# Optimization experiments

Hardware: AMD Instinct MI355X
Metric: run time of the kernel (lower is better)

The kernel has to match this reference:

```python
import jax, jax.numpy as jnp
import numpy as np

DIM = 1024
HEADS = 16


def setup_inputs() -> dict:
    key = jax.random.key(0)
    k1, k2, k3, k4 = jax.random.split(key, 4)
    x = jax.random.normal(k1, (4, 2048, DIM), dtype=jnp.float32)
    s = 1.0 / np.sqrt(DIM)
    w_qkv = jax.random.normal(k2, (DIM, 3 * DIM), dtype=jnp.float32) * s
    w_out = jax.random.normal(k3, (DIM, DIM), dtype=jnp.float32) * s
    b_out = jax.random.normal(k4, (DIM,), dtype=jnp.float32) * 0.01
    return {"x": x, "w_qkv": w_qkv, "w_out": w_out, "b_out": b_out}


def reference(x, w_qkv, w_out, b_out):
    b, n, d = x.shape
    h = HEADS
    dh = d // h
    scale = dh ** -0.5
    qkv = x @ w_qkv  # [b, n, 3d]
    q, k, v = jnp.split(qkv, 3, axis=-1)
    # [b, n, d] -> [b, h, n, dh]
    def to_heads(t):
        return t.reshape(b, n, h, dh).transpose(0, 2, 1, 3)
    q, k, v = to_heads(q), to_heads(k), to_heads(v)
    dots = jnp.einsum('bhid,bhjd->bhij', q, k) * scale
    attn = jax.nn.softmax(dots, axis=-1)
    out = jnp.einsum('bhij,bhjd->bhid', attn, v)
    out = out.transpose(0, 2, 1, 3).reshape(b, n, d)
    return out @ w_out + b_out
```

## Files before the change

kernel.cpp:

```cpp
#include <hip/hip_runtime.h>
#include <hip/hip_bf16.h>


typedef __attribute__((ext_vector_type(4))) float f32x4;
typedef __attribute__((ext_vector_type(16))) float f32x16;
typedef __attribute__((ext_vector_type(8))) unsigned short u16x8;
typedef __attribute__((ext_vector_type(4))) unsigned short u16x4;
typedef __attribute__((ext_vector_type(4))) unsigned int u32x4;
typedef __attribute__((ext_vector_type(8))) __bf16 bf16x8;

static __device__ __forceinline__ f32x4 mfma_bf16(u16x8 a, u16x8 b, f32x4 c) {
    return __builtin_amdgcn_mfma_f32_16x16x32_bf16(
        __builtin_bit_cast(bf16x8, a), __builtin_bit_cast(bf16x8, b), c, 0, 0, 0);
}
static __device__ __forceinline__ f32x16 mfma32(u16x8 a, u16x8 b, f32x16 c) {
    return __builtin_amdgcn_mfma_f32_32x32x16_bf16(
        __builtin_bit_cast(bf16x8, a), __builtin_bit_cast(bf16x8, b), c, 0, 0, 0);
}

static __device__ __forceinline__ unsigned short f2bf(float f) {
    unsigned int u = __builtin_bit_cast(unsigned int, f);
    u += 0x7fffu + ((u >> 16) & 1u);
    return (unsigned short)(u >> 16);
}
static __device__ __forceinline__ unsigned int cvt_pk_bf16(float a, float b) {
    unsigned int r;
    asm("v_cvt_pk_bf16_f32 %0, %1, %2" : "=v"(r) : "v"(a), "v"(b));
    return r;
}
static __device__ __forceinline__ float fexp2(float x) {
    float r;
    asm("v_exp_f32 %0, %1" : "=v"(r) : "v"(x));
    return r;
}
static __device__ __forceinline__ float frcp(float x) {
    float r;
    asm("v_rcp_f32 %0, %1" : "=v"(r) : "v"(x));
    return r;
}
typedef const __attribute__((address_space(1))) unsigned int* gp1_t;
typedef __attribute__((address_space(3))) unsigned int* lp3_t;
static __device__ __forceinline__ void gl_lds16(const void* g, void* l) {
    __builtin_amdgcn_global_load_lds((gp1_t)g, (lp3_t)l, 16, 0, 0);
}

__global__ void k_prep(const float* __restrict__ x, unsigned short* __restrict__ xb,
                       const float* __restrict__ w_qkv, unsigned short* __restrict__ wqkvT,
                       const float* __restrict__ w_out, unsigned short* __restrict__ woutT) {
    int blk = blockIdx.x, tid = threadIdx.x;
    if (blk < 2048) {
        int i = blk * 256 + tid;
        int stride = 2048 * 256;
        int n4 = 8192 * 1024 / 4;
        for (; i < n4; i += stride) {
            f32x4 v = ((const f32x4*)x)[i];
            u16x4 o;
            #pragma unroll
            for (int j = 0; j < 4; ++j) o[j] = f2bf(v[j]);
            ((u16x4*)xb)[i] = o;
        }
        return;
    }
    __shared__ float tile[32][33];
    const float* in; unsigned short* out; int R, C, scale_rows, c0, r0;
    float scale;
    if (blk < 5120) {
        int idx = blk - 2048;
        in = w_qkv; out = wqkvT; R = 1024; C = 3072;
        scale_rows = 1024; scale = 0.18033688f;
        c0 = (idx % 96) * 32; r0 = (idx / 96) * 32;
    } else {
        int idx = blk - 5120;
        in = w_out; out = woutT; R = 1024; C = 1024;
        scale_rows = 0; scale = 1.0f;
        c0 = (idx % 32) * 32; r0 = (idx / 32) * 32;
    }
    int tx = tid & 31, ty = tid >> 5;
    #pragma unroll
    for (int i = ty; i < 32; i += 8)
        tile[i][tx] = in[(size_t)(r0 + i) * C + c0 + tx];
    __syncthreads();
    #pragma unroll
    for (int i = ty; i < 32; i += 8) {
        float v = tile[tx][i];
        if (c0 + i < scale_rows) v *= scale;
        out[(size_t)(c0 + i) * R + r0 + tx] = f2bf(v);
    }
}

__global__ __launch_bounds__(512, 1) void k_gemm1f(
    const unsigned short* __restrict__ A,
    const unsigned short* __restrict__ BT,
    unsigned short* __restrict__ qkv,
    unsigned short* __restrict__ VTs)
{
    __shared__ unsigned short As[2][256 * 64];
    __shared__ unsigned short Bs[2][384 * 64];
    const int K = 1024;
    const int tid = threadIdx.x, lane = tid & 63, wave = tid >> 6;

    int lin = blockIdx.y * 8 + blockIdx.x;
    int xcd = lin & 7, idx = lin >> 3;
    int by = xcd * 4 + (idx >> 3);
    int bxg = idx & 7;
    const int m0 = by * 256, n0 = bxg * 384;

    const int wm = (wave >> 1) * 64, wn = (wave & 1) * 192;
    const int lr = lane & 15, half = lane >> 4;
    const int srow = lane >> 3, sslot = lane & 7;

    auto stage = [&](int buf, int t) {
        int k0 = t * 64;
        #pragma unroll
        for (int r = 0; r < 4; ++r) {
            int chunk = r * 8 + wave;
            int row = chunk * 8 + srow;
            int koff = (sslot ^ (row & 7)) * 8;
            gl_lds16(&A[(size_t)(m0 + row) * K + k0 + koff], &As[buf][chunk * 512]);
        }
        #pragma unroll
        for (int r = 0; r < 6; ++r) {
            int chunk = r * 8 + wave;
            int row = chunk * 8 + srow;
            int koff = (sslot ^ (row & 7)) * 8;
            gl_lds16(&BT[(size_t)(n0 + row) * K + k0 + koff], &Bs[buf][chunk * 512]);
        }
    };

    f32x4 acc[4][12] = {};

    stage(0, 0);
    asm volatile("s_waitcnt vmcnt(0)" ::: "memory");
    __builtin_amdgcn_s_barrier();

    for (int t = 0; t < 16; ++t) {
        const int cur = t & 1;
        if (t < 15) stage(cur ^ 1, t + 1);
        const unsigned short* Ab = As[cur];
        const unsigned short* Bb = Bs[cur];

        #pragma unroll
        for (int ks = 0; ks < 2; ++ks) {
            u16x8 af[4];
            #pragma unroll
            for (int i = 0; i < 4; ++i) {
                int ra = wm + i * 16 + lr;
                af[i] = *(const u16x8*)&Ab[ra * 64 + (((ks * 4 + half) ^ (ra & 7)) * 8)];
            }
            #pragma unroll
            for (int j = 0; j < 12; ++j) {
                int rb = wn + j * 16 + lr;
                u16x8 bfr = *(const u16x8*)&Bb[rb * 64 + (((ks * 4 + half) ^ (rb & 7)) * 8)];
                __builtin_amdgcn_s_setprio(1);
                #pragma unroll
                for (int i = 0; i < 4; ++i)
                    acc[i][j] = mfma_bf16(af[i], bfr, acc[i][j]);
                __builtin_amdgcn_s_setprio(0);
            }
        }

        asm volatile("s_waitcnt vmcnt(0) lgkmcnt(0)" ::: "memory");
        __builtin_amdgcn_s_barrier();
    }

    #pragma unroll
    for (int i = 0; i < 4; ++i) {
        int rowb = m0 + wm + i * 16 + half * 4;
        #pragma unroll
        for (int j = 0; j < 12; ++j) {
            int col = n0 + wn + j * 16 + lr;
            if (col < 2048) {
                #pragma unroll
                for (int r = 0; r < 4; ++r)
                    qkv[(size_t)(rowb + r) * 3072 + col] = f2bf(acc[i][j][r]);
            } else {
                int cj = col - 2048, h = cj >> 6, d = cj & 63;
                int b = rowb >> 11, n = rowb & 2047;
                u16x4 p;
                #pragma unroll
                for (int r = 0; r < 4; ++r) p[r] = f2bf(acc[i][j][r]);
                *(u16x4*)&VTs[((size_t)((b * 16 + h) * 64 + d)) * 2048 + n] = p;
            }
        }
    }
}

__global__ __launch_bounds__(512, 1) void k_gemm2(
    const unsigned short* __restrict__ A,
    const unsigned short* __restrict__ BT,
    const float* __restrict__ bias,
    float* __restrict__ outf)
{
    __shared__ unsigned short As[3][256 * 64];
    __shared__ unsigned short Bs[3][128 * 64];
    const int K = 1024;
    const int tid = threadIdx.x, lane = tid & 63, wave = tid >> 6;

    int lin = blockIdx.y * 8 + blockIdx.x;
    int virt = (lin & 7) * 32 + (lin >> 3);
    int bx = virt % 8, by = virt / 8;
    const int m0 = by * 256, n0 = bx * 128;

    const int wm = (wave >> 1) * 64, wn = (wave & 1) * 64;
    const int lr = lane & 15, half = lane >> 4;
    const int srow = lane >> 3, sslot = lane & 7;

    auto stage_sub = [&](int buf, int t, int h) {
        int k0 = t * 64;
        #pragma unroll
        for (int r = 0; r < 2; ++r) {
            int chunk = (h * 2 + r) * 8 + wave;
            int row = chunk * 8 + srow;
            int koff = (sslot ^ (row & 7)) * 8;
            gl_lds16(&A[(size_t)(m0 + row) * K + k0 + koff], &As[buf][chunk * 512]);
        }
        {
            int chunk = h * 8 + wave;
            int row = chunk * 8 + srow;
            int koff = (sslot ^ (row & 7)) * 8;
            gl_lds16(&BT[(size_t)(n0 + row) * K + k0 + koff], &Bs[buf][chunk * 512]);
        }
    };

    f32x4 acc[4][4] = {};

    stage_sub(0, 0, 0); stage_sub(0, 0, 1);
    stage_sub(1, 1, 0); stage_sub(1, 1, 1);
    asm volatile("s_waitcnt vmcnt(6)" ::: "memory");
    __builtin_amdgcn_s_barrier();

    for (int t = 0; t < 16; ++t) {
        const int cur = t % 3, nxt = (t + 2) % 3;
        const bool do_stage = (t + 2) < 16;
        const unsigned short* Ab = As[cur];
        const unsigned short* Bb = Bs[cur];

        #pragma unroll
        for (int ks = 0; ks < 2; ++ks) {
            u16x8 af[4], bfr[4];
            #pragma unroll
            for (int i = 0; i < 4; ++i) {
                int ra = wm + i * 16 + lr;
                af[i] = *(const u16x8*)&Ab[ra * 64 + (((ks * 4 + half) ^ (ra & 7)) * 8)];
                int rb = wn + i * 16 + lr;
                bfr[i] = *(const u16x8*)&Bb[rb * 64 + (((ks * 4 + half) ^ (rb & 7)) * 8)];
            }
            if (do_stage) stage_sub(nxt, t + 2, ks);
            if (ks == 1) {
                if (t < 14)       asm volatile("s_waitcnt vmcnt(6)" ::: "memory");
                else if (t == 14) asm volatile("s_waitcnt vmcnt(0)" ::: "memory");
            }
            __builtin_amdgcn_s_barrier();
            asm volatile("s_waitcnt lgkmcnt(0)" ::: "memory");
            __builtin_amdgcn_sched_barrier(0);
            __builtin_amdgcn_s_setprio(1);
            #pragma unroll
            for (int i = 0; i < 4; ++i)
                #pragma unroll
                for (int j = 0; j < 4; ++j)
                    acc[i][j] = mfma_bf16(af[i], bfr[j], acc[i][j]);
            __builtin_amdgcn_s_setprio(0);
            __builtin_amdgcn_s_barrier();
        }
    }

    #pragma unroll
    for (int i = 0; i < 4; ++i)
        #pragma unroll
        for (int j = 0; j < 4; ++j)
            #pragma unroll
            for (int r = 0; r < 4; ++r) {
                int row = m0 + wm + i * 16 + half * 4 + r;
                int col = n0 + wn + j * 16 + lr;
                outf[(size_t)row * 1024 + col] = acc[i][j][r] + bias[col];
            }
}

__global__ __launch_bounds__(256, 4) void k_attn(
    const unsigned short* __restrict__ qkv,
    const unsigned short* __restrict__ VTs,
    unsigned short* __restrict__ attn)
{
    __shared__ unsigned short Kt[2][64 * 64];
    __shared__ unsigned short Vt[2][64 * 64];
    const int tid = threadIdx.x, lane = tid & 63, wave = tid >> 6;

    int lin = blockIdx.y * 16 + blockIdx.x;
    int virt = (lin & 7) * 128 + (lin >> 3);
    int bh = virt >> 4;
    int q0 = (virt & 15) * 128 + wave * 32;

    const int lq = lane & 31;
    const int hi = lane >> 5;

    int b = bh >> 4, h = bh & 15;
    const unsigned short* Kq = qkv + (size_t)(b * 2048) * 3072 + 1024 + h * 64;
    const unsigned short* Vbase = VTs + (size_t)bh * 64 * 2048;

    u16x8 qf[4];
    {
        const unsigned short* Qr = qkv + (size_t)(b * 2048 + q0 + lq) * 3072 + h * 64;
        #pragma unroll
        for (int kk = 0; kk < 4; ++kk)
            qf[kk] = *(const u16x8*)&Qr[kk * 16 + hi * 8];
    }

    const int srow_in = lane >> 4, sslot = lane & 15;
    auto stage = [&](int buf, int j0) {
        #pragma unroll
        for (int c = 0; c < 2; ++c) {
            int chunk = wave * 2 + c;
            int row = chunk * 4 + srow_in;
            int v = sslot ^ (row & 15);
            int high = v >> 3, dsl = (v & 7) * 8;
            gl_lds16(Kq + (size_t)(j0 + high * 32 + row) * 3072 + dsl, &Kt[buf][chunk * 512]);
            gl_lds16(Vbase + (size_t)(high * 32 + row) * 2048 + j0 + dsl, &Vt[buf][chunk * 512]);
        }
    };

    f32x16 o[2] = {};
    f32x16 osum = {};
    const u16x8 onesf = {0x3F80, 0x3F80, 0x3F80, 0x3F80, 0x3F80, 0x3F80, 0x3F80, 0x3F80};

    stage(0, 0);
    __syncthreads();
    int cur = 0;

    for (int t = 0; t < 32; ++t) {
        if (t < 31) stage(cur ^ 1, (t + 1) * 64);

        f32x16 sacc[2] = {};
        __builtin_amdgcn_s_setprio(1);
        #pragma unroll
        for (int jb = 0; jb < 2; ++jb) {
            u16x8 kf[4];
            #pragma unroll
            for (int kk = 0; kk < 4; ++kk) {
                int s = (jb * 8 + kk * 2 + hi) ^ (lq & 15);
                kf[kk] = *(const u16x8*)&Kt[cur][lq * 128 + s * 8];
            }
            #pragma unroll
            for (int kk = 0; kk < 4; ++kk)
                sacc[jb] = mfma32(kf[kk], qf[kk], sacc[jb]);
        }
        __builtin_amdgcn_s_setprio(0);

        unsigned int pk[16];
        #pragma unroll
        for (int jb = 0; jb < 2; ++jb)
            #pragma unroll
            for (int i = 0; i < 8; ++i)
                pk[jb * 8 + i] = cvt_pk_bf16(fexp2(sacc[jb][2 * i]), fexp2(sacc[jb][2 * i + 1]));

        __builtin_amdgcn_s_setprio(1);
        #pragma unroll
        for (int kk = 0; kk < 4; ++kk) {
            const int base = (kk >> 1) * 8 + (kk & 1) * 4;
            unsigned int w0 = pk[base + 0], w2 = pk[base + 2];
            unsigned int w1 = pk[base + 1], w3 = pk[base + 3];
            asm("v_permlane32_swap_b32 %0, %1" : "+v"(w0), "+v"(w2));
            asm("v_permlane32_swap_b32 %0, %1" : "+v"(w1), "+v"(w3));
            u32x4 w; w[0] = w0; w[1] = w1; w[2] = w2; w[3] = w3;
            u16x8 pa = __builtin_bit_cast(u16x8, w);
            osum = mfma32(pa, onesf, osum);
            #pragma unroll
            for (int db = 0; db < 2; ++db) {
                int s = (db * 8 + kk * 2 + hi) ^ (lq & 15);
                u16x8 vf = *(const u16x8*)&Vt[cur][lq * 128 + s * 8];
                o[db] = mfma32(pa, vf, o[db]);
            }
        }
        __builtin_amdgcn_s_setprio(0);

        __syncthreads();
        cur ^= 1;
    }

    #pragma unroll
    for (int r = 0; r < 16; ++r) {
        int qrow = (r & 3) + 8 * (r >> 2) + 4 * hi;
        float invr = frcp(osum[r]);
        size_t ro = (size_t)(b * 2048 + q0 + qrow) * 1024 + h * 64;
        attn[ro + lq]      = f2bf(o[0][r] * invr);
        attn[ro + 32 + lq] = f2bf(o[1][r] * invr);
    }
}

extern "C" void kernel_launch(void* const* d_in, const int* in_sizes, int n_in,
                              void* d_out, int out_size, void* d_ws, size_t ws_size,
                              hipStream_t stream) {
    const float* x     = (const float*)d_in[0];
    const float* w_qkv = (const float*)d_in[1];
    const float* w_out = (const float*)d_in[2];
    const float* b_out = (const float*)d_in[3];
    float* out = (float*)d_out;

    char* ws = (char*)d_ws;
    size_t off = 0;
    auto alloc = [&](size_t bytes) -> void* {
        void* p = ws + off;
        off += (bytes + 255) & ~(size_t)255;
        return p;
    };
    unsigned short* xb    = (unsigned short*)alloc(8192ull * 1024 * 2);
    unsigned short* wqkvT = (unsigned short*)alloc(3072ull * 1024 * 2);
    unsigned short* woutT = (unsigned short*)alloc(1024ull * 1024 * 2);
    unsigned short* qkv   = (unsigned short*)alloc(8192ull * 3072 * 2);
    unsigned short* VTs   = (unsigned short*)alloc(64ull * 2048 * 64 * 2);
    if (off > ws_size) return;

    k_prep<<<6144, 256, 0, stream>>>(x, xb, w_qkv, wqkvT, w_out, woutT);
    k_gemm1f<<<dim3(8, 32), 512, 0, stream>>>(xb, wqkvT, qkv, VTs);
    k_attn<<<dim3(16, 64), 256, 0, stream>>>(qkv, VTs, xb);
    k_gemm2<<<dim3(8, 32), 512, 0, stream>>>(xb, woutT, b_out, out);
}
```

Baseline: 184.5 us.

## Process two 32-row query tiles per wave in attention to reuse K/V fragments

Each attention wave now handles 64 query rows as two independent 32-row tiles, so every K and V fragment read from LDS feeds two MFMAs. Blocks cover 256 query rows and the grid is halved. The aim is to cut LDS reads and global K/V staging per unit of work and to give the scheduler more independent MFMA chains. In exchange register pressure roughly doubles, occupancy drops from 4 to 2 blocks per CU, and fewer blocks are available to fill the GPU.

```diff
diff --git a/kernel.cpp b/kernel.cpp
--- a/kernel.cpp
+++ b/kernel.cpp
@@ -276,7 +276,7 @@
             }
 }
 
-__global__ __launch_bounds__(256, 4) void k_attn(
+__global__ __launch_bounds__(256, 2) void k_attn(
     const unsigned short* __restrict__ qkv,
     const unsigned short* __restrict__ VTs,
     unsigned short* __restrict__ attn)
@@ -285,10 +285,10 @@
     __shared__ unsigned short Vt[2][64 * 64];
     const int tid = threadIdx.x, lane = tid & 63, wave = tid >> 6;
 
-    int lin = blockIdx.y * 16 + blockIdx.x;
-    int virt = (lin & 7) * 128 + (lin >> 3);
-    int bh = virt >> 4;
-    int q0 = (virt & 15) * 128 + wave * 32;
+    int lin = blockIdx.y * 8 + blockIdx.x;
+    int virt = (lin & 7) * 64 + (lin >> 3);
+    int bh = virt >> 3;
+    int q0 = (virt & 7) * 256 + wave * 64;
 
     const int lq = lane & 31;
     const int hi = lane >> 5;
@@ -297,12 +297,15 @@
     const unsigned short* Kq = qkv + (size_t)(b * 2048) * 3072 + 1024 + h * 64;
     const unsigned short* Vbase = VTs + (size_t)bh * 64 * 2048;
 
-    u16x8 qf[4];
+    u16x8 qfA[4], qfB[4];
     {
-        const unsigned short* Qr = qkv + (size_t)(b * 2048 + q0 + lq) * 3072 + h * 64;
-        #pragma unroll
-        for (int kk = 0; kk < 4; ++kk)
-            qf[kk] = *(const u16x8*)&Qr[kk * 16 + hi * 8];
+        const unsigned short* QrA = qkv + (size_t)(b * 2048 + q0 + lq) * 3072 + h * 64;
+        const unsigned short* QrB = QrA + 32 * 3072;
+        #pragma unroll
+        for (int kk = 0; kk < 4; ++kk) {
+            qfA[kk] = *(const u16x8*)&QrA[kk * 16 + hi * 8];
+            qfB[kk] = *(const u16x8*)&QrB[kk * 16 + hi * 8];
+        }
     }
 
     const int srow_in = lane >> 4, sslot = lane & 15;
@@ -318,8 +321,8 @@
         }
     };
 
-    f32x16 o[2] = {};
-    f32x16 osum = {};
+    f32x16 oA[2] = {}, oB[2] = {};
+    f32x16 osumA = {}, osumB = {};
     const u16x8 onesf = {0x3F80, 0x3F80, 0x3F80, 0x3F80, 0x3F80, 0x3F80, 0x3F80, 0x3F80};
 
     stage(0, 0);
@@ -329,7 +332,7 @@
     for (int t = 0; t < 32; ++t) {
         if (t < 31) stage(cur ^ 1, (t + 1) * 64);
 
-        f32x16 sacc[2] = {};
+        f32x16 sA[2] = {}, sB[2] = {};
         __builtin_amdgcn_s_setprio(1);
         #pragma unroll
         for (int jb = 0; jb < 2; ++jb) {
@@ -340,34 +343,49 @@
                 kf[kk] = *(const u16x8*)&Kt[cur][lq * 128 + s * 8];
             }
             #pragma unroll
-            for (int kk = 0; kk < 4; ++kk)
-                sacc[jb] = mfma32(kf[kk], qf[kk], sacc[jb]);
+            for (int kk = 0; kk < 4; ++kk) sA[jb] = mfma32(kf[kk], qfA[kk], sA[jb]);
+            #pragma unroll
+            for (int kk = 0; kk < 4; ++kk) sB[jb] = mfma32(kf[kk], qfB[kk], sB[jb]);
         }
         __builtin_amdgcn_s_setprio(0);
 
-        unsigned int pk[16];
-        #pragma unroll
-        for (int jb = 0; jb < 2; ++jb)
-            #pragma unroll
-            for (int i = 0; i < 8; ++i)
-                pk[jb * 8 + i] = cvt_pk_bf16(fexp2(sacc[jb][2 * i]), fexp2(sacc[jb][2 * i + 1]));
-
-        __builtin_amdgcn_s_setprio(1);
+        u16x8 paA[4], paB[4];
         #pragma unroll
         for (int kk = 0; kk < 4; ++kk) {
-            const int base = (kk >> 1) * 8 + (kk & 1) * 4;
-            unsigned int w0 = pk[base + 0], w2 = pk[base + 2];
-            unsigned int w1 = pk[base + 1], w3 = pk[base + 3];
+            const int jb = kk >> 1, e0 = (kk & 1) * 8;
+            unsigned int w0 = cvt_pk_bf16(fexp2(sA[jb][e0 + 0]), fexp2(sA[jb][e0 + 1]));
+            unsigned int w1 = cvt_pk_bf16(fexp2(sA[jb][e0 + 2]), fexp2(sA[jb][e0 + 3]));
+            unsigned int w2 = cvt_pk_bf16(fexp2(sA[jb][e0 + 4]), fexp2(sA[jb][e0 + 5]));
+            unsigned int w3 = cvt_pk_bf16(fexp2(sA[jb][e0 + 6]), fexp2(sA[jb][e0 + 7]));
             asm("v_permlane32_swap_b32 %0, %1" : "+v"(w0), "+v"(w2));
             asm("v_permlane32_swap_b32 %0, %1" : "+v"(w1), "+v"(w3));
             u32x4 w; w[0] = w0; w[1] = w1; w[2] = w2; w[3] = w3;
-            u16x8 pa = __builtin_bit_cast(u16x8, w);
-            osum = mfma32(pa, onesf, osum);
+            paA[kk] = __builtin_bit_cast(u16x8, w);
+        }
+        #pragma unroll
+        for (int kk = 0; kk < 4; ++kk) {
+            const int jb = kk >> 1, e0 = (kk & 1) * 8;
+            unsigned int w0 = cvt_pk_bf16(fexp2(sB[jb][e0 + 0]), fexp2(sB[jb][e0 + 1]));
+            unsigned int w1 = cvt_pk_bf16(fexp2(sB[jb][e0 + 2]), fexp2(sB[jb][e0 + 3]));
+            unsigned int w2 = cvt_pk_bf16(fexp2(sB[jb][e0 + 4]), fexp2(sB[jb][e0 + 5]));
+            unsigned int w3 = cvt_pk_bf16(fexp2(sB[jb][e0 + 6]), fexp2(sB[jb][e0 + 7]));
+            asm("v_permlane32_swap_b32 %0, %1" : "+v"(w0), "+v"(w2));
+            asm("v_permlane32_swap_b32 %0, %1" : "+v"(w1), "+v"(w3));
+            u32x4 w; w[0] = w0; w[1] = w1; w[2] = w2; w[3] = w3;
+            paB[kk] = __builtin_bit_cast(u16x8, w);
+        }
+
+        __builtin_amdgcn_s_setprio(1);
+        #pragma unroll
+        for (int kk = 0; kk < 4; ++kk) {
+            osumA = mfma32(paA[kk], onesf, osumA);
+            osumB = mfma32(paB[kk], onesf, osumB);
             #pragma unroll
             for (int db = 0; db < 2; ++db) {
                 int s = (db * 8 + kk * 2 + hi) ^ (lq & 15);
                 u16x8 vf = *(const u16x8*)&Vt[cur][lq * 128 + s * 8];
-                o[db] = mfma32(pa, vf, o[db]);
+                oA[db] = mfma32(paA[kk], vf, oA[db]);
+                oB[db] = mfma32(paB[kk], vf, oB[db]);
             }
         }
         __builtin_amdgcn_s_setprio(0);
@@ -379,10 +397,14 @@
     #pragma unroll
     for (int r = 0; r < 16; ++r) {
         int qrow = (r & 3) + 8 * (r >> 2) + 4 * hi;
-        float invr = frcp(osum[r]);
-        size_t ro = (size_t)(b * 2048 + q0 + qrow) * 1024 + h * 64;
-        attn[ro + lq]      = f2bf(o[0][r] * invr);
-        attn[ro + 32 + lq] = f2bf(o[1][r] * invr);
+        float iA = frcp(osumA[r]);
+        float iB = frcp(osumB[r]);
+        size_t roA = (size_t)(b * 2048 + q0 + qrow) * 1024 + h * 64;
+        size_t roB = (size_t)(b * 2048 + q0 + 32 + qrow) * 1024 + h * 64;
+        attn[roA + lq]      = f2bf(oA[0][r] * iA);
+        attn[roA + 32 + lq] = f2bf(oA[1][r] * iA);
+        attn[roB + lq]      = f2bf(oB[0][r] * iB);
+        attn[roB + 32 + lq] = f2bf(oB[1][r] * iB);
     }
 }
 
@@ -411,6 +433,6 @@
 
     k_prep<<<6144, 256, 0, stream>>>(x, xb, w_qkv, wqkvT, w_out, woutT);
     k_gemm1f<<<dim3(8, 32), 512, 0, stream>>>(xb, wqkvT, qkv, VTs);
-    k_attn<<<dim3(16, 64), 256, 0, stream>>>(qkv, VTs, xb);
+    k_attn<<<dim3(8, 64), 256, 0, stream>>>(qkv, VTs, xb);
     k_gemm2<<<dim3(8, 32), 512, 0, stream>>>(xb, woutT, b_out, out);
 }
```

Result: faster. 175.0 us (-5.1%).
